# Kernel tuning notes

Hardware: AMD Instinct MI355X
Metric: run time of the kernel (lower is better)

## Reference

```python
import jax, jax.numpy as jnp
import numpy as np

NUM_HEADS = 8
NUM_LANDMARKS = 64
TOPK_LANDMARKS = 4


def setup_inputs() -> dict:
    key = jax.random.key(0)
    k1, k2, k3, k4 = jax.random.split(key, 4)
    B, N, C = 1, 2048, 512
    return {
        "x": jax.random.normal(k1, (B, N, C), jnp.float32),
        "w_qkv": jax.random.normal(k2, (3 * C, C), jnp.float32) * 0.02,
        "w_proj": jax.random.normal(k3, (C, C), jnp.float32) * 0.02,
        "b_proj": jax.random.normal(k4, (C,), jnp.float32) * 0.02,
    }


def reference(x, w_qkv, w_proj, b_proj):
    B, N, C = x.shape
    H = NUM_HEADS
    Dh = C // H
    m = min(NUM_LANDMARKS, N)          # number of segments (torch views (B,H,m,seg,D))
    kl = min(TOPK_LANDMARKS, m)
    scale = Dh ** -0.5

    qkv = (x @ w_qkv.T).reshape(B, N, 3, H, Dh).transpose(2, 0, 3, 1, 4)
    q, k, v = qkv[0], qkv[1], qkv[2]   # each (B,H,N,Dh)

    seg = -(-N // m)                   # segment length = ceil(N/m)
    pad = seg * m - N

    def segmentize(t):
        if pad > 0:
            t = jnp.pad(t, ((0, 0), (0, 0), (0, pad), (0, 0)))
        return t.reshape(B, H, m, seg, Dh)

    k_seg = segmentize(k)              # (B,H,m,seg,Dh)
    v_seg = segmentize(v)

    centroids = k_seg.mean(axis=3)     # (B,H,m,Dh) -- includes pad zeros, as in torch
    route = jnp.einsum('bhnd,bhmd->bhnm', q, centroids) * scale
    _, topk_idx = jax.lax.top_k(route, kl)  # (B,H,N,kl)

    # gather routed segments per query: (B,H,N,kl,seg,Dh)
    gather = jax.vmap(jax.vmap(lambda segs, ix: segs[ix]))
    sel_k = gather(k_seg, topk_idx).reshape(B, H, N, kl * seg, Dh)
    sel_v = gather(v_seg, topk_idx).reshape(B, H, N, kl * seg, Dh)

    attn = jnp.einsum('bhnd,bhnkd->bhnk', q, sel_k) * scale
    attn = jax.nn.softmax(attn, axis=-1)
    out = jnp.einsum('bhnk,bhnkd->bhnd', attn, sel_v)  # (B,H,N,Dh)
    out = out.transpose(0, 2, 1, 3).reshape(B, N, C)
    return out @ w_proj.T + b_proj
```

## Files before the change

kernel.cpp:

```cpp
#include <hip/hip_runtime.h>
#include <hip/hip_bf16.h>
#include <math.h>

#define N_TOK 2048
#define C_DIM 512
#define H_NUM 8
#define DH 64
#define M_LM 64
#define SEG 32
#define KL 4
#define SCALE 0.125f

typedef __attribute__((ext_vector_type(8))) short short8;
typedef __attribute__((ext_vector_type(4))) float f32x4;

__device__ inline unsigned short f2bf(float f) {
  unsigned u = __float_as_uint(f);
  u += 0x7FFF + ((u >> 16) & 1);
  return (unsigned short)(u >> 16);
}
__device__ inline float bf2f(unsigned short h) {
  return __uint_as_float(((unsigned)h) << 16);
}

__global__ __launch_bounds__(256) void gemm_qk(
    const float* __restrict__ A, const float* __restrict__ B,
    float* __restrict__ out_q, float* __restrict__ out_k)
{
  __shared__ float As[32][68];
  __shared__ float Bs[32][68];
  int tid = threadIdx.x;
  int tx = tid & 15, ty = tid >> 4;
  int row0 = blockIdx.y << 6;
  int col0 = blockIdx.x << 6;
  float acc[4][4] = {};
  int kk = tid & 31, rr = tid >> 5;

  float pa[8], pb[8];
#pragma unroll
  for (int i = 0; i < 8; i++) {
    pa[i] = A[(size_t)(row0 + rr + i * 8) * 512 + kk];
    pb[i] = B[(size_t)(col0 + rr + i * 8) * 512 + kk];
  }

  for (int k0 = 0; k0 < 512; k0 += 32) {
    __syncthreads();
#pragma unroll
    for (int i = 0; i < 8; i++) {
      As[kk][rr + i * 8] = pa[i];
      Bs[kk][rr + i * 8] = pb[i];
    }
    __syncthreads();
    if (k0 + 32 < 512) {
#pragma unroll
      for (int i = 0; i < 8; i++) {
        pa[i] = A[(size_t)(row0 + rr + i * 8) * 512 + k0 + 32 + kk];
        pb[i] = B[(size_t)(col0 + rr + i * 8) * 512 + k0 + 32 + kk];
      }
    }
#pragma unroll
    for (int kk2 = 0; kk2 < 32; kk2++) {
      float a[4], b[4];
      *(float4*)a = *(const float4*)&As[kk2][ty << 2];
      *(float4*)b = *(const float4*)&Bs[kk2][tx << 2];
#pragma unroll
      for (int i = 0; i < 4; i++)
#pragma unroll
        for (int j = 0; j < 4; j++) acc[i][j] += a[i] * b[j];
    }
  }

  int t = col0 >> 9;
  int h = (col0 >> 6) & 7;
  float* dst = (t == 0) ? out_q : out_k;
#pragma unroll
  for (int i = 0; i < 4; i++) {
    int n = row0 + (ty << 2) + i;
#pragma unroll
    for (int j = 0; j < 4; j++) {
      int d = (tx << 2) + j;
      dst[(size_t)((h << 11) + n) * DH + d] = acc[i][j];
    }
  }
}

__global__ void split3_kernel(const float* __restrict__ x, const float* __restrict__ wv,
                              const float* __restrict__ wp,
                              unsigned short* __restrict__ X2,
                              unsigned short* __restrict__ W2v,
                              unsigned short* __restrict__ WP2)
{
  int idx = blockIdx.x * 256 + threadIdx.x;
  const float* src; unsigned short* dst; int li;
  if (idx < 1048576)      { src = x;  dst = X2;  li = idx; }
  else if (idx < 1310720) { src = wv; dst = W2v; li = idx - 1048576; }
  else                    { src = wp; dst = WP2; li = idx - 1310720; }
  int r = li >> 9, k = li & 511;
  float a = src[li];
  unsigned short h1 = f2bf(a);
  float r1 = a - bf2f(h1);
  dst[(size_t)(r << 10) + k] = h1;
  dst[(size_t)(r << 10) + 512 + k] = f2bf(r1);
}

__global__ __launch_bounds__(256) void gemm_mfma(
    const unsigned short* __restrict__ A2, const unsigned short* __restrict__ B2,
    float* __restrict__ ov, float* __restrict__ ofull,
    const float* __restrict__ bias, int ldout, int mode)
{
  __shared__ short Al[4096];
  __shared__ short Bl[4096];
  int tid = threadIdx.x;
  int lane = tid & 63, w = tid >> 6;
  int row0 = blockIdx.y << 6, col0 = blockIdx.x << 6;
  int wr = (w >> 1) * 32, wc = (w & 1) * 32;
  int m_lo = tid & 7, h8 = (tid >> 3) & 7, m_hi = tid >> 6;
  int ms = m_hi * 8 + m_lo;
  int q = lane >> 4, ln = lane & 15;

  f32x4 acc[2][2];
#pragma unroll
  for (int mi = 0; mi < 2; mi++)
#pragma unroll
    for (int ni = 0; ni < 2; ni++)
#pragma unroll
      for (int r = 0; r < 4; r++) acc[mi][ni][r] = 0.0f;

  for (int s = 0; s < 24; s++) {
    int ka = (s < 8) ? s * 64 : (s < 16) ? 512 + (s - 8) * 64 : (s - 16) * 64;
    int kb = (s < 8) ? s * 64 : (s < 16) ? (s - 8) * 64 : 512 + (s - 16) * 64;
    short8 a0 = *(const short8*)(A2 + (size_t)(row0 + ms) * 1024 + ka + h8 * 8);
    short8 a1 = *(const short8*)(A2 + (size_t)(row0 + ms + 32) * 1024 + ka + h8 * 8);
    short8 b0 = *(const short8*)(B2 + (size_t)(col0 + ms) * 1024 + kb + h8 * 8);
    short8 b1 = *(const short8*)(B2 + (size_t)(col0 + ms + 32) * 1024 + kb + h8 * 8);
    __syncthreads();
    *(short8*)&Al[(h8 * 64 + ms) * 8] = a0;
    *(short8*)&Al[(h8 * 64 + ms + 32) * 8] = a1;
    *(short8*)&Bl[(h8 * 64 + ms) * 8] = b0;
    *(short8*)&Bl[(h8 * 64 + ms + 32) * 8] = b1;
    __syncthreads();
    short8 af[2][2], bf[2][2];
#pragma unroll
    for (int sub = 0; sub < 2; sub++)
#pragma unroll
      for (int i = 0; i < 2; i++) {
        af[sub][i] = *(const short8*)&Al[((sub * 4 + q) * 64 + wr + i * 16 + ln) * 8];
        bf[sub][i] = *(const short8*)&Bl[((sub * 4 + q) * 64 + wc + i * 16 + ln) * 8];
      }
#pragma unroll
    for (int sub = 0; sub < 2; sub++)
#pragma unroll
      for (int mi = 0; mi < 2; mi++)
#pragma unroll
        for (int ni = 0; ni < 2; ni++)
          acc[mi][ni] = __builtin_amdgcn_mfma_f32_16x16x32_bf16(
              af[sub][mi], bf[sub][ni], acc[mi][ni], 0, 0, 0);
  }

  if (mode == 0) {
    int hh = (col0 >> 6) & 7;
#pragma unroll
    for (int mi = 0; mi < 2; mi++)
#pragma unroll
      for (int ni = 0; ni < 2; ni++)
#pragma unroll
        for (int r = 0; r < 4; r++) {
          int row = row0 + wr + mi * 16 + q * 4 + r;
          int d = wc + ni * 16 + ln;
          ov[(size_t)((hh << 11) + row) * DH + d] = acc[mi][ni][r];
        }
  } else {
#pragma unroll
    for (int mi = 0; mi < 2; mi++)
#pragma unroll
      for (int ni = 0; ni < 2; ni++)
#pragma unroll
        for (int r = 0; r < 4; r++) {
          int row = row0 + wr + mi * 16 + q * 4 + r;
          int col = col0 + wc + ni * 16 + ln;
          ofull[(size_t)row * ldout + col] = acc[mi][ni][r] + bias[col];
        }
  }
}

__global__ void centroid_kernel(const float* __restrict__ kb, float* __restrict__ cent)
{
  int idx = blockIdx.x * blockDim.x + threadIdx.x;
  int m = (idx >> 6) & 63;
  int h = idx >> 12;
  int d = idx & 63;
  const float* base = kb + ((size_t)(h << 11) + m * SEG) * DH + d;
  float s = 0.f;
#pragma unroll
  for (int ss = 0; ss < SEG; ss++) s += base[(size_t)ss * DH];
  cent[idx] = s * (1.0f / SEG);
}

__global__ __launch_bounds__(256) void route_topk_kernel(
    const float* __restrict__ qb, const float* __restrict__ cent, int* __restrict__ topk)
{
  __shared__ float centT[64][65];
  __shared__ float qs[4][64];
  int tid = threadIdx.x;
  int wave = tid >> 6, lane = tid & 63;
  int qi = (blockIdx.x << 2) + wave;
  int h = qi >> 11;
  qs[wave][lane] = qb[(size_t)qi * DH + lane];
  const float4* c4 = (const float4*)(cent + ((size_t)h << 12));
#pragma unroll
  for (int i = 0; i < 4; i++) {
    int f4 = tid + 256 * i;
    int m = f4 >> 4;
    int d0 = (f4 & 15) * 4;
    float4 v = c4[f4];
    centT[d0][m] = v.x; centT[d0 + 1][m] = v.y;
    centT[d0 + 2][m] = v.z; centT[d0 + 3][m] = v.w;
  }
  __syncthreads();
  float dot = 0.f;
#pragma unroll
  for (int d = 0; d < 64; d++) dot += qs[wave][d] * centT[d][lane];
  float val = dot * SCALE;
  for (int r = 0; r < KL; r++) {
    float v = val;
    int id = lane;
#pragma unroll
    for (int off = 32; off; off >>= 1) {
      float ov = __shfl_xor(v, off, 64);
      int oi = __shfl_xor(id, off, 64);
      if (ov > v || (ov == v && oi < id)) { v = ov; id = oi; }
    }
    if (lane == 0) topk[qi * KL + r] = id;
    if (lane == id) val = -INFINITY;
  }
}

__global__ __launch_bounds__(256) void attn_kernel(
    const float* __restrict__ qb, const float* __restrict__ kb,
    const float* __restrict__ vb, const int* __restrict__ topk,
    unsigned short* __restrict__ ao2)
{
  __shared__ float probs[4][128];
  int tid = threadIdx.x;
  int wave = tid >> 6, lane = tid & 63;
  int qi = (blockIdx.x << 2) + wave;
  int h = qi >> 11, n = qi & 2047;
  int4 tk = *(const int4*)(topk + qi * KL);
  int segArr[4] = {tk.x, tk.y, tk.z, tk.w};
  const float* qrow = qb + (size_t)qi * DH;
  float4 qreg[4];
#pragma unroll
  for (int i = 0; i < 4; i++)
    qreg[i] = *(const float4*)(qrow + ((lane & 3) + 4 * i) * 4);

  float e[8];
  float score[8];
#pragma unroll
  for (int g = 0; g < 8; g++) {
    int seg = segArr[g >> 1];
    int key_n = seg * SEG + (lane >> 2) + 16 * (g & 1);
    const float* krow = kb + ((size_t)(h << 11) + key_n) * DH;
    float acc = 0.f;
#pragma unroll
    for (int i = 0; i < 4; i++) {
      float4 kv = *(const float4*)(krow + ((lane & 3) + 4 * i) * 4);
      float4 qv = qreg[i];
      acc += qv.x * kv.x + qv.y * kv.y + qv.z * kv.z + qv.w * kv.w;
    }
    acc += __shfl_xor(acc, 1, 64);
    acc += __shfl_xor(acc, 2, 64);
    score[g] = acc * SCALE;
  }
  float mx = score[0];
#pragma unroll
  for (int g = 1; g < 8; g++) mx = fmaxf(mx, score[g]);
#pragma unroll
  for (int off = 4; off < 64; off <<= 1) mx = fmaxf(mx, __shfl_xor(mx, off, 64));
  float ls = 0.f;
#pragma unroll
  for (int g = 0; g < 8; g++) { e[g] = expf(score[g] - mx); ls += e[g]; }
#pragma unroll
  for (int off = 4; off < 64; off <<= 1) ls += __shfl_xor(ls, off, 64);
  float inv = 1.0f / ls;
  if ((lane & 3) == 0) {
#pragma unroll
    for (int g = 0; g < 8; g++) probs[wave][(lane >> 2) + 16 * g] = e[g] * inv;
  }
  __syncthreads();

  float o = 0.f;
#pragma unroll
  for (int si = 0; si < KL; si++) {
    int seg = segArr[si];
    const float* vrow = vb + ((size_t)(h << 11) + seg * SEG) * DH + lane;
#pragma unroll
    for (int ss = 0; ss < SEG; ss++) o += probs[wave][(si << 5) + ss] * vrow[(size_t)ss * DH];
  }
  unsigned short hb = f2bf(o);
  float lo = o - bf2f(hb);
  ao2[(size_t)n * 1024 + (h << 6) + lane] = hb;
  ao2[(size_t)n * 1024 + 512 + (h << 6) + lane] = f2bf(lo);
}

extern "C" void kernel_launch(void* const* d_in, const int* in_sizes, int n_in,
                              void* d_out, int out_size, void* d_ws, size_t ws_size,
                              hipStream_t stream)
{
  const float* x      = (const float*)d_in[0];
  const float* w_qkv  = (const float*)d_in[1];
  const float* w_proj = (const float*)d_in[2];
  const float* b_proj = (const float*)d_in[3];
  float* out = (float*)d_out;

  float* base = (float*)d_ws;
  float* qbuf = base;
  float* kbuf = base + 1048576;
  float* vbuf = base + 2097152;
  float* cent = base + 3145728;
  int*   topk = (int*)(base + 3178496);
  unsigned short* X2  = (unsigned short*)(base + 3244032);
  unsigned short* W2v = (unsigned short*)(base + 4292608);
  unsigned short* WP2 = (unsigned short*)(base + 4554752);
  unsigned short* AO2 = X2;

  split3_kernel<<<6144, 256, 0, stream>>>(x, w_qkv + 1024 * 512, w_proj,
                                          X2, W2v, WP2);
  {
    dim3 grid(1024 / 64, N_TOK / 64);
    gemm_qk<<<grid, 256, 0, stream>>>(x, w_qkv, qbuf, kbuf);
  }
  {
    dim3 grid(512 / 64, N_TOK / 64);
    gemm_mfma<<<grid, 256, 0, stream>>>(X2, W2v, vbuf, nullptr, nullptr, 0, 0);
  }
  centroid_kernel<<<(H_NUM * M_LM * DH) / 256, 256, 0, stream>>>(kbuf, cent);
  route_topk_kernel<<<(H_NUM * N_TOK) / 4, 256, 0, stream>>>(qbuf, cent, topk);
  attn_kernel<<<(H_NUM * N_TOK) / 4, 256, 0, stream>>>(qbuf, kbuf, vbuf, topk, AO2);
  {
    dim3 grid(C_DIM / 64, N_TOK / 64);
    gemm_mfma<<<grid, 256, 0, stream>>>(AO2, WP2, nullptr, out, b_proj, C_DIM, 1);
  }
}
```

Baseline: 209.3 us.

## Split PV accumulation across segments per lane with float4 V loads

```diff
diff --git a/kernel.cpp b/kernel.cpp
--- a/kernel.cpp
+++ b/kernel.cpp
@@ -240,7 +240,7 @@
     const float* __restrict__ vb, const int* __restrict__ topk,
     unsigned short* __restrict__ ao2)
 {
-  __shared__ float probs[4][128];
+  __shared__ float probs[4][132];
   int tid = threadIdx.x;
   int wave = tid >> 6, lane = tid & 63;
   int qi = (blockIdx.x << 2) + wave;
@@ -260,13 +260,17 @@
     int seg = segArr[g >> 1];
     int key_n = seg * SEG + (lane >> 2) + 16 * (g & 1);
     const float* krow = kb + ((size_t)(h << 11) + key_n) * DH;
-    float acc = 0.f;
+    float4 a4 = {0.f, 0.f, 0.f, 0.f};
 #pragma unroll
     for (int i = 0; i < 4; i++) {
       float4 kv = *(const float4*)(krow + ((lane & 3) + 4 * i) * 4);
       float4 qv = qreg[i];
-      acc += qv.x * kv.x + qv.y * kv.y + qv.z * kv.z + qv.w * kv.w;
-    }
+      a4.x += qv.x * kv.x;
+      a4.y += qv.y * kv.y;
+      a4.z += qv.z * kv.z;
+      a4.w += qv.w * kv.w;
+    }
+    float acc = (a4.x + a4.y) + (a4.z + a4.w);
     acc += __shfl_xor(acc, 1, 64);
     acc += __shfl_xor(acc, 2, 64);
     score[g] = acc * SCALE;
@@ -284,22 +288,56 @@
   float inv = 1.0f / ls;
   if ((lane & 3) == 0) {
 #pragma unroll
-    for (int g = 0; g < 8; g++) probs[wave][(lane >> 2) + 16 * g] = e[g] * inv;
+    for (int g = 0; g < 8; g++)
+      probs[wave][(g >> 1) * 33 + (lane >> 2) + 16 * (g & 1)] = e[g] * inv;
   }
   __syncthreads();
 
-  float o = 0.f;
-#pragma unroll
-  for (int si = 0; si < KL; si++) {
-    int seg = segArr[si];
-    const float* vrow = vb + ((size_t)(h << 11) + seg * SEG) * DH + lane;
-#pragma unroll
-    for (int ss = 0; ss < SEG; ss++) o += probs[wave][(si << 5) + ss] * vrow[(size_t)ss * DH];
-  }
-  unsigned short hb = f2bf(o);
-  float lo = o - bf2f(hb);
-  ao2[(size_t)n * 1024 + (h << 6) + lane] = hb;
-  ao2[(size_t)n * 1024 + 512 + (h << 6) + lane] = f2bf(lo);
+  int gi = lane >> 4, lx = lane & 15;
+  int seg = segArr[gi];
+  const float4* v4 = (const float4*)(vb + ((size_t)(h << 11) + seg * SEG) * DH);
+  float4 oa = {0.f, 0.f, 0.f, 0.f};
+  float4 ob = {0.f, 0.f, 0.f, 0.f};
+  float4 oc = {0.f, 0.f, 0.f, 0.f};
+  float4 od = {0.f, 0.f, 0.f, 0.f};
+#pragma unroll
+  for (int ss = 0; ss < SEG; ss += 4) {
+    float p0 = probs[wave][gi * 33 + ss];
+    float p1 = probs[wave][gi * 33 + ss + 1];
+    float p2 = probs[wave][gi * 33 + ss + 2];
+    float p3 = probs[wave][gi * 33 + ss + 3];
+    float4 v0 = v4[(ss + 0) * 16 + lx];
+    float4 v1 = v4[(ss + 1) * 16 + lx];
+    float4 v2 = v4[(ss + 2) * 16 + lx];
+    float4 v3 = v4[(ss + 3) * 16 + lx];
+    oa.x += p0 * v0.x; oa.y += p0 * v0.y; oa.z += p0 * v0.z; oa.w += p0 * v0.w;
+    ob.x += p1 * v1.x; ob.y += p1 * v1.y; ob.z += p1 * v1.z; ob.w += p1 * v1.w;
+    oc.x += p2 * v2.x; oc.y += p2 * v2.y; oc.z += p2 * v2.z; oc.w += p2 * v2.w;
+    od.x += p3 * v3.x; od.y += p3 * v3.y; od.z += p3 * v3.z; od.w += p3 * v3.w;
+  }
+  float4 o4;
+  o4.x = (oa.x + ob.x) + (oc.x + od.x);
+  o4.y = (oa.y + ob.y) + (oc.y + od.y);
+  o4.z = (oa.z + ob.z) + (oc.z + od.z);
+  o4.w = (oa.w + ob.w) + (oc.w + od.w);
+#pragma unroll
+  for (int off = 16; off < 64; off <<= 1) {
+    o4.x += __shfl_xor(o4.x, off, 64);
+    o4.y += __shfl_xor(o4.y, off, 64);
+    o4.z += __shfl_xor(o4.z, off, 64);
+    o4.w += __shfl_xor(o4.w, off, 64);
+  }
+  if (lane < 16) {
+    unsigned short hx = f2bf(o4.x), hy = f2bf(o4.y), hz = f2bf(o4.z), hw = f2bf(o4.w);
+    ushort4 hi4, lo4;
+    hi4.x = hx; hi4.y = hy; hi4.z = hz; hi4.w = hw;
+    lo4.x = f2bf(o4.x - bf2f(hx));
+    lo4.y = f2bf(o4.y - bf2f(hy));
+    lo4.z = f2bf(o4.z - bf2f(hz));
+    lo4.w = f2bf(o4.w - bf2f(hw));
+    *(ushort4*)(ao2 + (size_t)n * 1024 + (h << 6) + (lane << 2)) = hi4;
+    *(ushort4*)(ao2 + (size_t)n * 1024 + 512 + (h << 6) + (lane << 2)) = lo4;
+  }
 }
 
 extern "C" void kernel_launch(void* const* d_in, const int* in_sizes, int n_in,
```

Measured after the change: 210.4 us. About the same (+0.5%).

## Store K and V in bf16 and vectorize attention PV accumulation

Applied to the files above, without the earlier changes.

```diff
diff --git a/kernel.cpp b/kernel.cpp
--- a/kernel.cpp
+++ b/kernel.cpp
@@ -12,6 +12,7 @@
 #define SCALE 0.125f
 
 typedef __attribute__((ext_vector_type(8))) short short8;
+typedef __attribute__((ext_vector_type(8))) unsigned short ushort8v;
 typedef __attribute__((ext_vector_type(4))) float f32x4;
 
 __device__ inline unsigned short f2bf(float f) {
@@ -105,7 +106,7 @@
 
 __global__ __launch_bounds__(256) void gemm_mfma(
     const unsigned short* __restrict__ A2, const unsigned short* __restrict__ B2,
-    float* __restrict__ ov, float* __restrict__ ofull,
+    unsigned short* __restrict__ ov16, float* __restrict__ ofull,
     const float* __restrict__ bias, int ldout, int mode)
 {
   __shared__ short Al[4096];
@@ -167,7 +168,7 @@
         for (int r = 0; r < 4; r++) {
           int row = row0 + wr + mi * 16 + q * 4 + r;
           int d = wc + ni * 16 + ln;
-          ov[(size_t)((hh << 11) + row) * DH + d] = acc[mi][ni][r];
+          ov16[(size_t)((hh << 11) + row) * DH + d] = f2bf(acc[mi][ni][r]);
         }
   } else {
 #pragma unroll
@@ -194,6 +195,15 @@
 #pragma unroll
   for (int ss = 0; ss < SEG; ss++) s += base[(size_t)ss * DH];
   cent[idx] = s * (1.0f / SEG);
+}
+
+__global__ void kbf_kernel(const float* __restrict__ kb, unsigned short* __restrict__ kbf)
+{
+  int idx = blockIdx.x * 256 + threadIdx.x;
+  float4 v = ((const float4*)kb)[idx];
+  ushort4 o;
+  o.x = f2bf(v.x); o.y = f2bf(v.y); o.z = f2bf(v.z); o.w = f2bf(v.w);
+  ((ushort4*)kbf)[idx] = o;
 }
 
 __global__ __launch_bounds__(256) void route_topk_kernel(
@@ -236,11 +246,11 @@
 }
 
 __global__ __launch_bounds__(256) void attn_kernel(
-    const float* __restrict__ qb, const float* __restrict__ kb,
-    const float* __restrict__ vb, const int* __restrict__ topk,
+    const float* __restrict__ qb, const unsigned short* __restrict__ kbf,
+    const unsigned short* __restrict__ vbf, const int* __restrict__ topk,
     unsigned short* __restrict__ ao2)
 {
-  __shared__ float probs[4][128];
+  __shared__ float probs[4][132];
   int tid = threadIdx.x;
   int wave = tid >> 6, lane = tid & 63;
   int qi = (blockIdx.x << 2) + wave;
@@ -250,8 +260,10 @@
   const float* qrow = qb + (size_t)qi * DH;
   float4 qreg[4];
 #pragma unroll
-  for (int i = 0; i < 4; i++)
-    qreg[i] = *(const float4*)(qrow + ((lane & 3) + 4 * i) * 4);
+  for (int j = 0; j < 2; j++) {
+    qreg[j * 2]     = *(const float4*)(qrow + ((lane & 3) + 4 * j) * 8);
+    qreg[j * 2 + 1] = *(const float4*)(qrow + ((lane & 3) + 4 * j) * 8 + 4);
+  }
 
   float e[8];
   float score[8];
@@ -259,14 +271,18 @@
   for (int g = 0; g < 8; g++) {
     int seg = segArr[g >> 1];
     int key_n = seg * SEG + (lane >> 2) + 16 * (g & 1);
-    const float* krow = kb + ((size_t)(h << 11) + key_n) * DH;
-    float acc = 0.f;
-#pragma unroll
-    for (int i = 0; i < 4; i++) {
-      float4 kv = *(const float4*)(krow + ((lane & 3) + 4 * i) * 4);
-      float4 qv = qreg[i];
-      acc += qv.x * kv.x + qv.y * kv.y + qv.z * kv.z + qv.w * kv.w;
-    }
+    const unsigned short* krow = kbf + ((size_t)(h << 11) + key_n) * DH;
+    float a0 = 0.f, a1 = 0.f, a2 = 0.f, a3 = 0.f;
+#pragma unroll
+    for (int j = 0; j < 2; j++) {
+      ushort8v kv = *(const ushort8v*)(krow + ((lane & 3) + 4 * j) * 8);
+      float4 q0 = qreg[j * 2], q1 = qreg[j * 2 + 1];
+      a0 += q0.x * bf2f(kv[0]); a1 += q0.y * bf2f(kv[1]);
+      a2 += q0.z * bf2f(kv[2]); a3 += q0.w * bf2f(kv[3]);
+      a0 += q1.x * bf2f(kv[4]); a1 += q1.y * bf2f(kv[5]);
+      a2 += q1.z * bf2f(kv[6]); a3 += q1.w * bf2f(kv[7]);
+    }
+    float acc = (a0 + a1) + (a2 + a3);
     acc += __shfl_xor(acc, 1, 64);
     acc += __shfl_xor(acc, 2, 64);
     score[g] = acc * SCALE;
@@ -284,22 +300,40 @@
   float inv = 1.0f / ls;
   if ((lane & 3) == 0) {
 #pragma unroll
-    for (int g = 0; g < 8; g++) probs[wave][(lane >> 2) + 16 * g] = e[g] * inv;
+    for (int g = 0; g < 8; g++)
+      probs[wave][(g >> 1) * 33 + (lane >> 2) + 16 * (g & 1)] = e[g] * inv;
   }
   __syncthreads();
 
-  float o = 0.f;
-#pragma unroll
-  for (int si = 0; si < KL; si++) {
-    int seg = segArr[si];
-    const float* vrow = vb + ((size_t)(h << 11) + seg * SEG) * DH + lane;
-#pragma unroll
-    for (int ss = 0; ss < SEG; ss++) o += probs[wave][(si << 5) + ss] * vrow[(size_t)ss * DH];
-  }
-  unsigned short hb = f2bf(o);
-  float lo = o - bf2f(hb);
-  ao2[(size_t)n * 1024 + (h << 6) + lane] = hb;
-  ao2[(size_t)n * 1024 + 512 + (h << 6) + lane] = f2bf(lo);
+  int gi = lane >> 4, lx = lane & 15;
+  int rh = lx >> 3, dl = lx & 7;
+  int seg = segArr[gi];
+  const unsigned short* vbase = vbf + ((size_t)(h << 11) + seg * SEG) * DH + dl * 8;
+  float o[8] = {};
+#pragma unroll
+  for (int ss = 0; ss < 16; ss++) {
+    int row = rh * 16 + ss;
+    float p = probs[wave][gi * 33 + row];
+    ushort8v vv = *(const ushort8v*)(vbase + (size_t)row * DH);
+#pragma unroll
+    for (int j = 0; j < 8; j++) o[j] += p * bf2f(vv[j]);
+  }
+#pragma unroll
+  for (int off = 8; off < 64; off <<= 1) {
+#pragma unroll
+    for (int j = 0; j < 8; j++) o[j] += __shfl_xor(o[j], off, 64);
+  }
+  if (lane < 8) {
+    ushort8v hi8, lo8;
+#pragma unroll
+    for (int j = 0; j < 8; j++) {
+      unsigned short hb = f2bf(o[j]);
+      hi8[j] = (short)hb;
+      lo8[j] = (short)f2bf(o[j] - bf2f(hb));
+    }
+    *(ushort8v*)(ao2 + (size_t)n * 1024 + (h << 6) + (lane << 3)) = hi8;
+    *(ushort8v*)(ao2 + (size_t)n * 1024 + 512 + (h << 6) + (lane << 3)) = lo8;
+  }
 }
 
 extern "C" void kernel_launch(void* const* d_in, const int* in_sizes, int n_in,
@@ -315,7 +349,8 @@
   float* base = (float*)d_ws;
   float* qbuf = base;
   float* kbuf = base + 1048576;
-  float* vbuf = base + 2097152;
+  unsigned short* vbf = (unsigned short*)(base + 2097152);
+  unsigned short* kbf = (unsigned short*)(base + 2097152 + 524288);
   float* cent = base + 3145728;
   int*   topk = (int*)(base + 3178496);
   unsigned short* X2  = (unsigned short*)(base + 3244032);
@@ -331,11 +366,12 @@
   }
   {
     dim3 grid(512 / 64, N_TOK / 64);
-    gemm_mfma<<<grid, 256, 0, stream>>>(X2, W2v, vbuf, nullptr, nullptr, 0, 0);
+    gemm_mfma<<<grid, 256, 0, stream>>>(X2, W2v, vbf, nullptr, nullptr, 0, 0);
   }
   centroid_kernel<<<(H_NUM * M_LM * DH) / 256, 256, 0, stream>>>(kbuf, cent);
+  kbf_kernel<<<1024, 256, 0, stream>>>(kbuf, kbf);
   route_topk_kernel<<<(H_NUM * N_TOK) / 4, 256, 0, stream>>>(qbuf, cent, topk);
-  attn_kernel<<<(H_NUM * N_TOK) / 4, 256, 0, stream>>>(qbuf, kbuf, vbuf, topk, AO2);
+  attn_kernel<<<(H_NUM * N_TOK) / 4, 256, 0, stream>>>(qbuf, kbf, vbf, topk, AO2);
   {
     dim3 grid(C_DIM / 64, N_TOK / 64);
     gemm_mfma<<<grid, 256, 0, stream>>>(AO2, WP2, nullptr, out, b_proj, C_DIM, 1);
```

Result: faster. 195.8 us (-6.4%).
